# Performance work log

Hardware: AMD Instinct MI355X
Metric: run time of the kernel (lower is better)

The kernel has to match this reference:

```python
import jax, jax.numpy as jnp
import numpy as np

N_NODES = 100000
N_EDGES = 3200000
IN_CH = 128
HID = 64
N_GRAPHS = 512


def _gcn_conv(x, W, b, src, dst, n_nodes):
    """PyG GCNConv: out = D^{-1/2} (A + I) D^{-1/2} X W + b.
    src/dst are edge endpoints; self-loops handled analytically."""
    h = x @ W  # [N, out]
    # degree with self-loops (count at target nodes, as in PyG)
    deg = jnp.zeros((n_nodes,), h.dtype).at[dst].add(1.0) + 1.0
    dis = jax.lax.rsqrt(deg)  # deg^{-1/2}
    norm = dis[src] * dis[dst]  # [E]
    msg = h[src] * norm[:, None]  # gather + scale, [E, out]
    out = jnp.zeros_like(h).at[dst].add(msg)  # scatter-add
    # self-loop term: norm_ii = 1/deg_i
    out = out + h * (dis * dis)[:, None]
    return out + b


def setup_inputs() -> dict:
    key = jax.random.key(0)
    ks = jax.random.split(key, 8)
    x = jax.random.normal(ks[0], (N_NODES, IN_CH), dtype=jnp.float32)
    edge_index = jax.random.randint(ks[1], (2, N_EDGES), 0, N_NODES, dtype=jnp.int64)
    batch = jnp.sort(jax.random.randint(ks[2], (N_NODES,), 0, N_GRAPHS, dtype=jnp.int64))
    s1 = 1.0 / np.sqrt(IN_CH)
    s2 = 1.0 / np.sqrt(HID)
    W1 = jax.random.uniform(ks[3], (IN_CH, HID), jnp.float32, -s1, s1)
    b1 = jax.random.uniform(ks[4], (HID,), jnp.float32, -s1, s1)
    W2 = jax.random.uniform(ks[5], (HID, HID), jnp.float32, -s2, s2)
    b2 = jax.random.uniform(ks[6], (HID,), jnp.float32, -s2, s2)
    return {"x": x, "edge_index": edge_index, "batch": batch,
            "W1": W1, "b1": b1, "W2": W2, "b2": b2}


def reference(x, edge_index, batch, W1, b1, W2, b2):
    src, dst = edge_index[0], edge_index[1]
    n = x.shape[0]
    h = jax.nn.relu(_gcn_conv(x, W1, b1, src, dst, n))
    h = jax.nn.relu(_gcn_conv(h, W2, b2, src, dst, n))
    # F.dropout(p=0.2) treated as identity (eval / deterministic reference)
    # global_mean_pool: segment mean over graph ids
    sums = jax.ops.segment_sum(h, batch, num_segments=N_GRAPHS)
    cnts = jax.ops.segment_sum(jnp.ones((n,), h.dtype), batch, num_segments=N_GRAPHS)
    return sums / jnp.maximum(cnts, 1.0)[:, None]
```

## Files before the change

### kernel.cpp

```cpp
#include <hip/hip_runtime.h>

typedef unsigned int uint;
typedef float f32x2 __attribute__((ext_vector_type(2)));

#define N_NODES 100000
#define N_EDGES 3200000
#define IN_CH 128
#define HID 64
#define N_GRAPHS 512
#define EPB 4096
#define NBLK ((N_EDGES + EPB - 1) / EPB)
#define NB 391
#define CAP 10240

__device__ __forceinline__ uint f2bf1(float f) {
    union { float f; uint i; } v; v.f = f;
    return (v.i + 0x7fffu + ((v.i >> 16) & 1u)) >> 16;
}
__device__ __forceinline__ uint pack2(float lo, float hi) {
    return f2bf1(lo) | (f2bf1(hi) << 16);
}
__device__ __forceinline__ float2 ub2(uint u) {
    union { uint i; float f; } a, b;
    a.i = u << 16; b.i = u & 0xffff0000u;
    return make_float2(a.f, b.f);
}
__device__ __forceinline__ f32x2 up2(uint u) {
    union { uint i; float f; } lo, hi;
    lo.i = u << 16; hi.i = u & 0xffff0000u;
    f32x2 r; r.x = lo.f; r.y = hi.f;
    return r;
}

__global__ __launch_bounds__(256) void scatter_kernel(const int* __restrict__ src,
                                                      const int* __restrict__ dst,
                                                      int* __restrict__ bcnt,
                                                      uint* __restrict__ pairs) {
    __shared__ int h[4 * NB];
    __shared__ int start[NB];
    __shared__ int cur[NB];
    int t = threadIdx.x;
    int base = blockIdx.x * EPB;

    int rs[16], rd[16];
#pragma unroll
    for (int j = 0; j < 16; ++j) {
        int e = base + j * 256 + t;
        if (e < N_EDGES) { rs[j] = src[e]; rd[j] = dst[e]; }
        else rd[j] = -1;
    }
    for (int i = t; i < 4 * NB; i += 256) h[i] = 0;
    __syncthreads();
    int w = t >> 6;
#pragma unroll
    for (int j = 0; j < 16; ++j)
        if (rd[j] >= 0) atomicAdd(&h[w * NB + (rd[j] >> 8)], 1);
    __syncthreads();
    for (int b = t; b < NB; b += 256) {
        int tot = h[b] + h[NB + b] + h[2 * NB + b] + h[3 * NB + b];
        start[b] = tot ? atomicAdd(&bcnt[b * 16], tot) : 0;
        cur[b] = 0;
    }
    __syncthreads();
#pragma unroll
    for (int j = 0; j < 16; ++j) {
        if (rd[j] >= 0) {
            int b = rd[j] >> 8;
            int r = atomicAdd(&cur[b], 1);
            pairs[(size_t)b * CAP + start[b] + r] =
                ((uint)(rd[j] & 255) << 24) | (uint)rs[j];
        }
    }
}

__global__ __launch_bounds__(512) void bucket_csr_kernel(const uint* __restrict__ pairs,
                                                         const int* __restrict__ bcnt,
                                                         int* __restrict__ csr_src,
                                                         int* __restrict__ rstart,
                                                         int* __restrict__ rend,
                                                         float* __restrict__ dis) {
    __shared__ int h8[8 * 256];
    __shared__ int h[256];
    int b = blockIdx.x;
    int t = threadIdx.x;
    int w = t >> 6;
    int e0 = b * CAP;
    int e1 = e0 + bcnt[b * 16];

    for (int i = t; i < 8 * 256; i += 512) h8[i] = 0;
    __syncthreads();

    int* hw = &h8[w * 256];
    int e = e0 + t;
    for (; e + 1536 < e1; e += 2048) {
        uint p0 = pairs[e], p1 = pairs[e + 512], p2 = pairs[e + 1024], p3 = pairs[e + 1536];
        atomicAdd(&hw[p0 >> 24], 1);
        atomicAdd(&hw[p1 >> 24], 1);
        atomicAdd(&hw[p2 >> 24], 1);
        atomicAdd(&hw[p3 >> 24], 1);
    }
    for (; e < e1; e += 512)
        atomicAdd(&hw[pairs[e] >> 24], 1);
    __syncthreads();

    int v = 0;
    if (t < 256) {
#pragma unroll
        for (int j = 0; j < 8; ++j) v += h8[j * 256 + t];
        h[t] = v;
    }
    __syncthreads();
#pragma unroll
    for (int o = 1; o < 256; o <<= 1) {
        int x = (t >= o && t < 256) ? h[t - o] : 0;
        __syncthreads();
        if (t < 256) h[t] += x;
        __syncthreads();
    }
    int excl = (t < 256) ? h[t] - v : 0;
    int n = b * 256 + t;
    if (t < 256 && n < N_NODES) {
        rstart[n] = e0 + excl;
        rend[n] = e0 + excl + v;
        dis[n] = rsqrtf((float)v + 1.0f);
    }
    __syncthreads();
    if (t < 256) h[t] = e0 + excl;
    __syncthreads();

    e = e0 + t;
    for (; e + 1536 < e1; e += 2048) {
        uint p0 = pairs[e], p1 = pairs[e + 512], p2 = pairs[e + 1024], p3 = pairs[e + 1536];
        int q0 = atomicAdd(&h[p0 >> 24], 1);
        int q1 = atomicAdd(&h[p1 >> 24], 1);
        int q2 = atomicAdd(&h[p2 >> 24], 1);
        int q3 = atomicAdd(&h[p3 >> 24], 1);
        csr_src[q0] = (int)(p0 & 0xFFFFFFu);
        csr_src[q1] = (int)(p1 & 0xFFFFFFu);
        csr_src[q2] = (int)(p2 & 0xFFFFFFu);
        csr_src[q3] = (int)(p3 & 0xFFFFFFu);
    }
    for (; e < e1; e += 512) {
        uint p = pairs[e];
        int pos = atomicAdd(&h[p >> 24], 1);
        csr_src[pos] = (int)(p & 0xFFFFFFu);
    }
}

__global__ __launch_bounds__(256) void gemm1_kernel(const float* __restrict__ X,
                                                    const float* __restrict__ W,
                                                    const float* __restrict__ dis,
                                                    uint* __restrict__ Y) {
    __shared__ float Wl[IN_CH * 64];
    __shared__ float Xs[128 * 33];
    int t = threadIdx.x;
    for (int idx = t; idx < IN_CH * 64; idx += 256) Wl[idx] = W[idx];

    int r0 = (t >> 3) * 4;
    int c0 = (t & 7) * 8;
    int rowBase = blockIdx.x * 128;

    float acc[4][8];
#pragma unroll
    for (int a = 0; a < 4; ++a)
#pragma unroll
        for (int c = 0; c < 8; ++c) acc[a][c] = 0.f;

    int srow = t >> 1;
    int shh = (t & 1) * 16;
    bool sok = (rowBase + srow) < N_NODES;
    const float* xbase = X + (size_t)(rowBase + srow) * IN_CH + shh;

    float4 nx[4];
#pragma unroll
    for (int f = 0; f < 4; ++f)
        nx[f] = sok ? *reinterpret_cast<const float4*>(xbase + f * 4)
                    : make_float4(0.f, 0.f, 0.f, 0.f);

    for (int kc = 0; kc < IN_CH; kc += 32) {
        if (kc) __syncthreads();
#pragma unroll
        for (int f = 0; f < 4; ++f) {
            int o = srow * 33 + shh + f * 4;
            Xs[o] = nx[f].x; Xs[o + 1] = nx[f].y; Xs[o + 2] = nx[f].z; Xs[o + 3] = nx[f].w;
        }
        __syncthreads();
        if (kc + 32 < IN_CH) {
#pragma unroll
            for (int f = 0; f < 4; ++f)
                nx[f] = sok ? *reinterpret_cast<const float4*>(xbase + kc + 32 + f * 4)
                            : make_float4(0.f, 0.f, 0.f, 0.f);
        }
#pragma unroll
        for (int kk = 0; kk < 32; ++kk) {
            const float4 wa = *reinterpret_cast<const float4*>(&Wl[(kc + kk) * 64 + c0]);
            const float4 wb = *reinterpret_cast<const float4*>(&Wl[(kc + kk) * 64 + c0 + 4]);
            float xr[4];
#pragma unroll
            for (int a = 0; a < 4; ++a) xr[a] = Xs[(r0 + a) * 33 + kk];
#pragma unroll
            for (int a = 0; a < 4; ++a) {
                acc[a][0] += xr[a] * wa.x; acc[a][1] += xr[a] * wa.y;
                acc[a][2] += xr[a] * wa.z; acc[a][3] += xr[a] * wa.w;
                acc[a][4] += xr[a] * wb.x; acc[a][5] += xr[a] * wb.y;
                acc[a][6] += xr[a] * wb.z; acc[a][7] += xr[a] * wb.w;
            }
        }
    }
#pragma unroll
    for (int a = 0; a < 4; ++a) {
        int row = rowBase + r0 + a;
        if (row < N_NODES) {
            float d = dis[row];
            uint4 o;
            o.x = pack2(acc[a][0] * d, acc[a][1] * d);
            o.y = pack2(acc[a][2] * d, acc[a][3] * d);
            o.z = pack2(acc[a][4] * d, acc[a][5] * d);
            o.w = pack2(acc[a][6] * d, acc[a][7] * d);
            *reinterpret_cast<uint4*>(Y + (size_t)row * 32 + (t & 7) * 4) = o;
        }
    }
}

__global__ __launch_bounds__(256) void gemm2_kernel(const uint* __restrict__ X,
                                                    const float* __restrict__ W,
                                                    const float* __restrict__ dis,
                                                    uint* __restrict__ Y) {
    __shared__ float Wl[HID * 64];
    __shared__ float Xs[128 * 33];
    int t = threadIdx.x;
    for (int idx = t; idx < HID * 64; idx += 256) Wl[idx] = W[idx];

    int r0 = (t >> 3) * 4;
    int c0 = (t & 7) * 8;
    int rowBase = blockIdx.x * 128;

    float acc[4][8];
#pragma unroll
    for (int a = 0; a < 4; ++a)
#pragma unroll
        for (int c = 0; c < 8; ++c) acc[a][c] = 0.f;

    int srow = t >> 1;
    int shh = (t & 1) * 16;
    bool sok = (rowBase + srow) < N_NODES;
    const uint* xbase = X + (size_t)(rowBase + srow) * 32 + (t & 1) * 8;

    uint4 n0_ = make_uint4(0, 0, 0, 0), n1_ = n0_;
    if (sok) {
        n0_ = *reinterpret_cast<const uint4*>(xbase);
        n1_ = *reinterpret_cast<const uint4*>(xbase + 4);
    }

    for (int kc = 0; kc < HID; kc += 32) {
        if (kc) __syncthreads();
        {
            uint us[8] = {n0_.x, n0_.y, n0_.z, n0_.w, n1_.x, n1_.y, n1_.z, n1_.w};
            int o = srow * 33 + shh;
#pragma unroll
            for (int j = 0; j < 8; ++j) {
                float2 f = ub2(us[j]);
                Xs[o + 2 * j]     = fmaxf(f.x, 0.f);
                Xs[o + 2 * j + 1] = fmaxf(f.y, 0.f);
            }
        }
        __syncthreads();
        if (kc + 32 < HID && sok) {
            n0_ = *reinterpret_cast<const uint4*>(xbase + 16);
            n1_ = *reinterpret_cast<const uint4*>(xbase + 20);
        }
#pragma unroll
        for (int kk = 0; kk < 32; ++kk) {
            const float4 wa = *reinterpret_cast<const float4*>(&Wl[(kc + kk) * 64 + c0]);
            const float4 wb = *reinterpret_cast<const float4*>(&Wl[(kc + kk) * 64 + c0 + 4]);
            float xr[4];
#pragma unroll
            for (int a = 0; a < 4; ++a) xr[a] = Xs[(r0 + a) * 33 + kk];
#pragma unroll
            for (int a = 0; a < 4; ++a) {
                acc[a][0] += xr[a] * wa.x; acc[a][1] += xr[a] * wa.y;
                acc[a][2] += xr[a] * wa.z; acc[a][3] += xr[a] * wa.w;
                acc[a][4] += xr[a] * wb.x; acc[a][5] += xr[a] * wb.y;
                acc[a][6] += xr[a] * wb.z; acc[a][7] += xr[a] * wb.w;
            }
        }
    }
#pragma unroll
    for (int a = 0; a < 4; ++a) {
        int row = rowBase + r0 + a;
        if (row < N_NODES) {
            float d = dis[row];
            uint4 o;
            o.x = pack2(acc[a][0] * d, acc[a][1] * d);
            o.y = pack2(acc[a][2] * d, acc[a][3] * d);
            o.z = pack2(acc[a][4] * d, acc[a][5] * d);
            o.w = pack2(acc[a][6] * d, acc[a][7] * d);
            *reinterpret_cast<uint4*>(Y + (size_t)row * 32 + (t & 7) * 4) = o;
        }
    }
}

__global__ __launch_bounds__(256) void gather_kernel(const int* __restrict__ rstart,
                                                     const int* __restrict__ rend,
                                                     const int* __restrict__ csr_src,
                                                     const float* __restrict__ dis,
                                                     const float* __restrict__ bias,
                                                     const uint* __restrict__ A,
                                                     uint* __restrict__ B) {
    int i = blockIdx.x * 4 + (threadIdx.x >> 6);
    if (i >= N_NODES) return;
    int lane = threadIdx.x & 63;
    int q = lane >> 3;
    int cu = (lane & 7) * 4;

    float4 bi0 = *reinterpret_cast<const float4*>(&bias[(lane & 7) * 8]);
    float4 bi1 = *reinterpret_cast<const float4*>(&bias[(lane & 7) * 8 + 4]);

    int e = rstart[i];
    int end = rend[i];

    f32x2 a[4], b[4];
#pragma unroll
    for (int j = 0; j < 4; ++j) { a[j] = (f32x2)0.f; b[j] = (f32x2)0.f; }

    if (q == 0) {
        uint4 u = *reinterpret_cast<const uint4*>(&A[(size_t)i * 32 + cu]);
        a[0] += up2(u.x); a[1] += up2(u.y); a[2] += up2(u.z); a[3] += up2(u.w);
    }
    for (; e + 16 <= end; e += 16) {
        int s0 = csr_src[e + q];
        int s1 = csr_src[e + 8 + q];
        uint4 u0 = *reinterpret_cast<const uint4*>(&A[(size_t)s0 * 32 + cu]);
        uint4 u1 = *reinterpret_cast<const uint4*>(&A[(size_t)s1 * 32 + cu]);
        a[0] += up2(u0.x); a[1] += up2(u0.y); a[2] += up2(u0.z); a[3] += up2(u0.w);
        b[0] += up2(u1.x); b[1] += up2(u1.y); b[2] += up2(u1.z); b[3] += up2(u1.w);
    }
    for (; e + 8 <= end; e += 8) {
        int s = csr_src[e + q];
        uint4 u = *reinterpret_cast<const uint4*>(&A[(size_t)s * 32 + cu]);
        a[0] += up2(u.x); a[1] += up2(u.y); a[2] += up2(u.z); a[3] += up2(u.w);
    }
    if (e + q < end) {
        int s = csr_src[e + q];
        uint4 u = *reinterpret_cast<const uint4*>(&A[(size_t)s * 32 + cu]);
        b[0] += up2(u.x); b[1] += up2(u.y); b[2] += up2(u.z); b[3] += up2(u.w);
    }
    float r[8];
#pragma unroll
    for (int j = 0; j < 4; ++j) {
        f32x2 s = a[j] + b[j];
        r[2 * j] = s.x; r[2 * j + 1] = s.y;
    }
#pragma unroll
    for (int j = 0; j < 8; ++j) {
        r[j] += __shfl_xor(r[j], 8);
        r[j] += __shfl_xor(r[j], 16);
        r[j] += __shfl_xor(r[j], 32);
    }
    if (q == 0) {
        float d = dis[i];
        uint4 o;
        o.x = pack2(bi0.x + d * r[0], bi0.y + d * r[1]);
        o.y = pack2(bi0.z + d * r[2], bi0.w + d * r[3]);
        o.z = pack2(bi1.x + d * r[4], bi1.y + d * r[5]);
        o.w = pack2(bi1.z + d * r[6], bi1.w + d * r[7]);
        *reinterpret_cast<uint4*>(B + (size_t)i * 32 + (lane & 7) * 4) = o;
    }
}

__global__ __launch_bounds__(256) void pool_kernel(const uint* __restrict__ B,
                                                   const int* __restrict__ batch,
                                                   float* __restrict__ sums,
                                                   float* __restrict__ cnt) {
    int w = blockIdx.x * 4 + (threadIdx.x >> 6);
    int half = (threadIdx.x >> 5) & 1;
    int l = threadIdx.x & 31;
    int n0 = w * 32 + half * 16;
    if (n0 >= N_NODES) return;
    int n1 = min(n0 + 16, N_NODES);
    int curg = batch[n0];
    float a0 = 0.f, a1 = 0.f;
    int run = 0;
    for (int n = n0; n < n1; ++n) {
        int g = batch[n];
        if (g != curg) {
            atomicAdd(&sums[curg * 64 + 2 * l], a0);
            atomicAdd(&sums[curg * 64 + 2 * l + 1], a1);
            if (l == 0) atomicAdd(&cnt[curg], (float)run);
            curg = g; a0 = 0.f; a1 = 0.f; run = 0;
        }
        float2 f = ub2(B[(size_t)n * 32 + l]);
        a0 += fmaxf(f.x, 0.f);
        a1 += fmaxf(f.y, 0.f);
        run++;
    }
    atomicAdd(&sums[curg * 64 + 2 * l], a0);
    atomicAdd(&sums[curg * 64 + 2 * l + 1], a1);
    if (l == 0) atomicAdd(&cnt[curg], (float)run);
}

__global__ __launch_bounds__(256) void final_kernel(const float* __restrict__ sums,
                                                    const float* __restrict__ cnt,
                                                    float* __restrict__ out) {
    int idx = blockIdx.x * 256 + threadIdx.x;
    if (idx < N_GRAPHS * 64) out[idx] = sums[idx] / fmaxf(cnt[idx >> 6], 1.0f);
}

extern "C" void kernel_launch(void* const* d_in, const int* in_sizes, int n_in,
                              void* d_out, int out_size, void* d_ws, size_t ws_size,
                              hipStream_t stream) {
    const float* x     = (const float*)d_in[0];
    const int*   edge  = (const int*)d_in[1];
    const int*   batch = (const int*)d_in[2];
    const float* W1    = (const float*)d_in[3];
    const float* b1    = (const float*)d_in[4];
    const float* W2    = (const float*)d_in[5];
    const float* b2    = (const float*)d_in[6];
    float* out = (float*)d_out;

    uint*  A        = (uint*)d_ws;
    uint*  B        = A + (size_t)N_NODES * 32;
    uint*  pairs    = B + (size_t)N_NODES * 32;
    int*   csr_src  = (int*)(pairs + (size_t)NB * CAP);
    float* dis      = (float*)(csr_src + (size_t)NB * CAP);
    int*   rstart   = (int*)(dis + N_NODES);
    int*   rend     = rstart + N_NODES;
    float* sums     = (float*)(rend + N_NODES);
    float* cnt_f    = sums + (size_t)N_GRAPHS * 64;
    int*   bcnt     = (int*)(cnt_f + N_GRAPHS);

    const int* src = edge;
    const int* dst = edge + N_EDGES;

    hipMemsetAsync(sums, 0, (N_GRAPHS * 64 + N_GRAPHS + NB * 16) * sizeof(float), stream);

    scatter_kernel<<<NBLK, 256, 0, stream>>>(src, dst, bcnt, pairs);
    bucket_csr_kernel<<<NB, 512, 0, stream>>>(pairs, bcnt, csr_src, rstart, rend, dis);

    gemm1_kernel<<<(N_NODES + 127) / 128, 256, 0, stream>>>(x, W1, dis, A);
    gather_kernel<<<(N_NODES + 3) / 4, 256, 0, stream>>>(rstart, rend, csr_src, dis, b1, A, B);

    gemm2_kernel<<<(N_NODES + 127) / 128, 256, 0, stream>>>(B, W2, dis, A);
    gather_kernel<<<(N_NODES + 3) / 4, 256, 0, stream>>>(rstart, rend, csr_src, dis, b2, A, B);

    pool_kernel<<<(N_NODES + 127) / 128, 256, 0, stream>>>(B, batch, sums, cnt_f);
    final_kernel<<<(N_GRAPHS * 64 + 255) / 256, 256, 0, stream>>>(sums, cnt_f, out);
}
```

Measured before the change: 358.7 us.

## Sub-sort CSR neighbor lists into four source-range bins per node

The bucket CSR build now sorts each destination's incoming edges into four sub-bins keyed on two bits of the source index (bits 15-16), and stores four segment starts per node. The gather kernel walks each of the four segments in order. The aim is to make neighbor-row fetches hit nearby addresses and improve cache locality in the gather. In exchange it adds 16KB more shared histogram state, an extra int4 boundary load per node, and more tail iterations per node in the gather loop.

```diff
diff --git a/kernel.cpp b/kernel.cpp
--- a/kernel.cpp
+++ b/kernel.cpp
@@ -31,6 +31,9 @@
     f32x2 r; r.x = lo.f; r.y = hi.f;
     return r;
 }
+__device__ __forceinline__ int binidx(uint p) {
+    return (int)(((p >> 24) << 2) | ((p >> 15) & 3u));
+}
 
 __global__ __launch_bounds__(256) void scatter_kernel(const int* __restrict__ src,
                                                       const int* __restrict__ dst,
@@ -76,65 +79,76 @@
 __global__ __launch_bounds__(512) void bucket_csr_kernel(const uint* __restrict__ pairs,
                                                          const int* __restrict__ bcnt,
                                                          int* __restrict__ csr_src,
-                                                         int* __restrict__ rstart,
+                                                         int* __restrict__ bnd4,
                                                          int* __restrict__ rend,
                                                          float* __restrict__ dis) {
-    __shared__ int h8[8 * 256];
-    __shared__ int h[256];
+    __shared__ int h8[8 * 1024];
+    __shared__ int hc[1024];
+    __shared__ int hn[256];
     int b = blockIdx.x;
     int t = threadIdx.x;
     int w = t >> 6;
     int e0 = b * CAP;
     int e1 = e0 + bcnt[b * 16];
 
-    for (int i = t; i < 8 * 256; i += 512) h8[i] = 0;
-    __syncthreads();
-
-    int* hw = &h8[w * 256];
+    for (int i = t; i < 8 * 1024; i += 512) h8[i] = 0;
+    __syncthreads();
+
+    int* hw = &h8[w * 1024];
     int e = e0 + t;
     for (; e + 1536 < e1; e += 2048) {
         uint p0 = pairs[e], p1 = pairs[e + 512], p2 = pairs[e + 1024], p3 = pairs[e + 1536];
-        atomicAdd(&hw[p0 >> 24], 1);
-        atomicAdd(&hw[p1 >> 24], 1);
-        atomicAdd(&hw[p2 >> 24], 1);
-        atomicAdd(&hw[p3 >> 24], 1);
+        atomicAdd(&hw[binidx(p0)], 1);
+        atomicAdd(&hw[binidx(p1)], 1);
+        atomicAdd(&hw[binidx(p2)], 1);
+        atomicAdd(&hw[binidx(p3)], 1);
     }
     for (; e < e1; e += 512)
-        atomicAdd(&hw[pairs[e] >> 24], 1);
+        atomicAdd(&hw[binidx(pairs[e])], 1);
+    __syncthreads();
+
+    for (int i = t; i < 1024; i += 512) {
+        int s = 0;
+#pragma unroll
+        for (int j = 0; j < 8; ++j) s += h8[j * 1024 + i];
+        hc[i] = s;
+    }
     __syncthreads();
 
     int v = 0;
     if (t < 256) {
-#pragma unroll
-        for (int j = 0; j < 8; ++j) v += h8[j * 256 + t];
-        h[t] = v;
+        v = hc[4 * t] + hc[4 * t + 1] + hc[4 * t + 2] + hc[4 * t + 3];
+        hn[t] = v;
     }
     __syncthreads();
 #pragma unroll
     for (int o = 1; o < 256; o <<= 1) {
-        int x = (t >= o && t < 256) ? h[t - o] : 0;
+        int x = (t >= o && t < 256) ? hn[t - o] : 0;
         __syncthreads();
-        if (t < 256) h[t] += x;
+        if (t < 256) hn[t] += x;
         __syncthreads();
     }
-    int excl = (t < 256) ? h[t] - v : 0;
-    int n = b * 256 + t;
-    if (t < 256 && n < N_NODES) {
-        rstart[n] = e0 + excl;
-        rend[n] = e0 + excl + v;
-        dis[n] = rsqrtf((float)v + 1.0f);
-    }
-    __syncthreads();
-    if (t < 256) h[t] = e0 + excl;
+    if (t < 256) {
+        int base = e0 + hn[t] - v;
+        int c0 = hc[4 * t], c1 = hc[4 * t + 1], c2 = hc[4 * t + 2];
+        int s0 = base, s1 = base + c0, s2 = s1 + c1, s3 = s2 + c2;
+        hc[4 * t] = s0; hc[4 * t + 1] = s1; hc[4 * t + 2] = s2; hc[4 * t + 3] = s3;
+        int n = b * 256 + t;
+        if (n < N_NODES) {
+            *reinterpret_cast<int4*>(&bnd4[(size_t)n * 4]) = make_int4(s0, s1, s2, s3);
+            rend[n] = base + v;
+            dis[n] = rsqrtf((float)v + 1.0f);
+        }
+    }
     __syncthreads();
 
     e = e0 + t;
     for (; e + 1536 < e1; e += 2048) {
         uint p0 = pairs[e], p1 = pairs[e + 512], p2 = pairs[e + 1024], p3 = pairs[e + 1536];
-        int q0 = atomicAdd(&h[p0 >> 24], 1);
-        int q1 = atomicAdd(&h[p1 >> 24], 1);
-        int q2 = atomicAdd(&h[p2 >> 24], 1);
-        int q3 = atomicAdd(&h[p3 >> 24], 1);
+        int q0 = atomicAdd(&hc[binidx(p0)], 1);
+        int q1 = atomicAdd(&hc[binidx(p1)], 1);
+        int q2 = atomicAdd(&hc[binidx(p2)], 1);
+        int q3 = atomicAdd(&hc[binidx(p3)], 1);
         csr_src[q0] = (int)(p0 & 0xFFFFFFu);
         csr_src[q1] = (int)(p1 & 0xFFFFFFu);
         csr_src[q2] = (int)(p2 & 0xFFFFFFu);
@@ -142,7 +156,7 @@
     }
     for (; e < e1; e += 512) {
         uint p = pairs[e];
-        int pos = atomicAdd(&h[p >> 24], 1);
+        int pos = atomicAdd(&hc[binidx(p)], 1);
         csr_src[pos] = (int)(p & 0xFFFFFFu);
     }
 }
@@ -300,7 +314,7 @@
     }
 }
 
-__global__ __launch_bounds__(256) void gather_kernel(const int* __restrict__ rstart,
+__global__ __launch_bounds__(256) void gather_kernel(const int* __restrict__ bnd4,
                                                      const int* __restrict__ rend,
                                                      const int* __restrict__ csr_src,
                                                      const float* __restrict__ dis,
@@ -316,8 +330,9 @@
     float4 bi0 = *reinterpret_cast<const float4*>(&bias[(lane & 7) * 8]);
     float4 bi1 = *reinterpret_cast<const float4*>(&bias[(lane & 7) * 8 + 4]);
 
-    int e = rstart[i];
-    int end = rend[i];
+    int4 bb = *reinterpret_cast<const int4*>(&bnd4[(size_t)i * 4]);
+    int st[4] = {bb.x, bb.y, bb.z, bb.w};
+    int en[4] = {bb.y, bb.z, bb.w, rend[i]};
 
     f32x2 a[4], b[4];
 #pragma unroll
@@ -327,23 +342,27 @@
         uint4 u = *reinterpret_cast<const uint4*>(&A[(size_t)i * 32 + cu]);
         a[0] += up2(u.x); a[1] += up2(u.y); a[2] += up2(u.z); a[3] += up2(u.w);
     }
-    for (; e + 16 <= end; e += 16) {
-        int s0 = csr_src[e + q];
-        int s1 = csr_src[e + 8 + q];
-        uint4 u0 = *reinterpret_cast<const uint4*>(&A[(size_t)s0 * 32 + cu]);
-        uint4 u1 = *reinterpret_cast<const uint4*>(&A[(size_t)s1 * 32 + cu]);
-        a[0] += up2(u0.x); a[1] += up2(u0.y); a[2] += up2(u0.z); a[3] += up2(u0.w);
-        b[0] += up2(u1.x); b[1] += up2(u1.y); b[2] += up2(u1.z); b[3] += up2(u1.w);
-    }
-    for (; e + 8 <= end; e += 8) {
-        int s = csr_src[e + q];
-        uint4 u = *reinterpret_cast<const uint4*>(&A[(size_t)s * 32 + cu]);
-        a[0] += up2(u.x); a[1] += up2(u.y); a[2] += up2(u.z); a[3] += up2(u.w);
-    }
-    if (e + q < end) {
-        int s = csr_src[e + q];
-        uint4 u = *reinterpret_cast<const uint4*>(&A[(size_t)s * 32 + cu]);
-        b[0] += up2(u.x); b[1] += up2(u.y); b[2] += up2(u.z); b[3] += up2(u.w);
+#pragma unroll
+    for (int g = 0; g < 4; ++g) {
+        int e = st[g], end = en[g];
+        for (; e + 16 <= end; e += 16) {
+            int s0 = csr_src[e + q];
+            int s1 = csr_src[e + 8 + q];
+            uint4 u0 = *reinterpret_cast<const uint4*>(&A[(size_t)s0 * 32 + cu]);
+            uint4 u1 = *reinterpret_cast<const uint4*>(&A[(size_t)s1 * 32 + cu]);
+            a[0] += up2(u0.x); a[1] += up2(u0.y); a[2] += up2(u0.z); a[3] += up2(u0.w);
+            b[0] += up2(u1.x); b[1] += up2(u1.y); b[2] += up2(u1.z); b[3] += up2(u1.w);
+        }
+        for (; e + 8 <= end; e += 8) {
+            int s = csr_src[e + q];
+            uint4 u = *reinterpret_cast<const uint4*>(&A[(size_t)s * 32 + cu]);
+            a[0] += up2(u.x); a[1] += up2(u.y); a[2] += up2(u.z); a[3] += up2(u.w);
+        }
+        if (e + q < end) {
+            int s = csr_src[e + q];
+            uint4 u = *reinterpret_cast<const uint4*>(&A[(size_t)s * 32 + cu]);
+            b[0] += up2(u.x); b[1] += up2(u.y); b[2] += up2(u.z); b[3] += up2(u.w);
+        }
     }
     float r[8];
 #pragma unroll
@@ -423,8 +442,8 @@
     uint*  pairs    = B + (size_t)N_NODES * 32;
     int*   csr_src  = (int*)(pairs + (size_t)NB * CAP);
     float* dis      = (float*)(csr_src + (size_t)NB * CAP);
-    int*   rstart   = (int*)(dis + N_NODES);
-    int*   rend     = rstart + N_NODES;
+    int*   bnd4     = (int*)(dis + N_NODES);
+    int*   rend     = bnd4 + (size_t)N_NODES * 4;
     float* sums     = (float*)(rend + N_NODES);
     float* cnt_f    = sums + (size_t)N_GRAPHS * 64;
     int*   bcnt     = (int*)(cnt_f + N_GRAPHS);
@@ -435,13 +454,13 @@
     hipMemsetAsync(sums, 0, (N_GRAPHS * 64 + N_GRAPHS + NB * 16) * sizeof(float), stream);
 
     scatter_kernel<<<NBLK, 256, 0, stream>>>(src, dst, bcnt, pairs);
-    bucket_csr_kernel<<<NB, 512, 0, stream>>>(pairs, bcnt, csr_src, rstart, rend, dis);
+    bucket_csr_kernel<<<NB, 512, 0, stream>>>(pairs, bcnt, csr_src, bnd4, rend, dis);
 
     gemm1_kernel<<<(N_NODES + 127) / 128, 256, 0, stream>>>(x, W1, dis, A);
-    gather_kernel<<<(N_NODES + 3) / 4, 256, 0, stream>>>(rstart, rend, csr_src, dis, b1, A, B);
+    gather_kernel<<<(N_NODES + 3) / 4, 256, 0, stream>>>(bnd4, rend, csr_src, dis, b1, A, B);
 
     gemm2_kernel<<<(N_NODES + 127) / 128, 256, 0, stream>>>(B, W2, dis, A);
-    gather_kernel<<<(N_NODES + 3) / 4, 256, 0, stream>>>(rstart, rend, csr_src, dis, b2, A, B);
+    gather_kernel<<<(N_NODES + 3) / 4, 256, 0, stream>>>(bnd4, rend, csr_src, dis, b2, A, B);
 
     pool_kernel<<<(N_NODES + 127) / 128, 256, 0, stream>>>(B, batch, sums, cnt_f);
     final_kernel<<<(N_GRAPHS * 64 + 255) / 256, 256, 0, stream>>>(sums, cnt_f, out);
```

New measurement: 403.9 us. +12.6%, slower.
